# Kernel optimization log

Hardware: AMD Instinct MI355X
Metric: run time of the kernel (lower is better)

The kernel has to match this reference:

```python
import math
import jax, jax.numpy as jnp
import numpy as np

V, D, DEPTH, H, DH, FF = 32000, 1024, 4, 16, 64, 4096
B, N = 1, 2048


def setup_inputs() -> dict:
    key = jax.random.key(0)
    ks = jax.random.split(key, 8)
    s = 0.02
    return {
        "x": jax.random.randint(ks[0], (B, N), 0, V, dtype=jnp.int32),
        "token_emb": jax.random.normal(ks[1], (V, D), jnp.float32) * s,
        "attn_gamma": jnp.ones((DEPTH, D), jnp.float32),
        "w_qkv": jax.random.normal(ks[2], (DEPTH, D, 3 * H * DH), jnp.float32) * s,
        "w_attn_out": jax.random.normal(ks[3], (DEPTH, H * DH, D), jnp.float32) * s,
        "ff_gamma": jnp.ones((DEPTH, D), jnp.float32),
        "w_ff1": jax.random.normal(ks[4], (DEPTH, D, FF), jnp.float32) * s,
        "b_ff1": jnp.zeros((DEPTH, FF), jnp.float32),
        "w_ff2": jax.random.normal(ks[5], (DEPTH, FF, D), jnp.float32) * s,
        "b_ff2": jnp.zeros((DEPTH, D), jnp.float32),
        "final_gamma": jnp.ones((D,), jnp.float32),
        "w_logits": jax.random.normal(ks[6], (D, V), jnp.float32) * s,
    }


def rms_norm(x, gamma):
    # F.normalize(x, dim=-1) * sqrt(D) * gamma
    norm = jnp.sqrt(jnp.sum(x * x, axis=-1, keepdims=True))
    return x / jnp.maximum(norm, 1e-12) * (x.shape[-1] ** 0.5) * gamma


def rope_cos_sin(n, dh, dtype):
    # lucidrains rotary-embedding-torch default: interleaved pairs
    inv_freq = 1.0 / (10000.0 ** (jnp.arange(0, dh, 2, dtype=jnp.float32) / dh))
    freqs = jnp.arange(n, dtype=jnp.float32)[:, None] * inv_freq[None, :]  # [n, dh/2]
    freqs = jnp.repeat(freqs, 2, axis=-1)  # [n, dh]
    return jnp.cos(freqs).astype(dtype), jnp.sin(freqs).astype(dtype)


def rotate_half(x):
    x1 = x[..., 0::2]
    x2 = x[..., 1::2]
    return jnp.stack((-x2, x1), axis=-1).reshape(x.shape)


def apply_rope(t, cos, sin):
    # t: [b, h, n, dh]; cos/sin: [n, dh]
    return t * cos[None, None] + rotate_half(t) * sin[None, None]


def decoder_forward(x, token_emb, attn_gamma, w_qkv, w_attn_out, ff_gamma,
                    w_ff1, b_ff1, w_ff2, b_ff2, final_gamma, w_logits):
    b, n = x.shape
    h = token_emb[x]  # [b, n, D]
    cos, sin = rope_cos_sin(n, DH, h.dtype)
    causal = jnp.triu(jnp.ones((n, n), bool), k=1)
    scale = DH ** -0.5
    neg = -jnp.finfo(h.dtype).max
    for l in range(DEPTH):
        # attention block
        xn = rms_norm(h, attn_gamma[l])
        qkv = xn @ w_qkv[l]  # [b, n, 3*H*DH]
        qkv = qkv.reshape(b, n, 3, H, DH).transpose(2, 0, 3, 1, 4)  # [3, b, H, n, DH]
        q, k, v = qkv[0], qkv[1], qkv[2]
        q = apply_rope(q, cos, sin)
        k = apply_rope(k, cos, sin)
        sim = jnp.einsum('bhid,bhjd->bhij', q, k) * scale
        sim = jnp.where(causal, neg, sim)
        attn = jax.nn.softmax(sim, axis=-1)
        out = jnp.einsum('bhij,bhjd->bhid', attn, v)
        out = out.transpose(0, 2, 1, 3).reshape(b, n, H * DH) @ w_attn_out[l]
        h = h + out
        # feedforward block
        fn = rms_norm(h, ff_gamma[l])
        ff = jax.nn.gelu(fn @ w_ff1[l] + b_ff1[l], approximate=False) @ w_ff2[l] + b_ff2[l]
        h = h + ff
    return rms_norm(h, final_gamma) @ w_logits


def reference(x, token_emb, attn_gamma, w_qkv, w_attn_out, ff_gamma,
              w_ff1, b_ff1, w_ff2, b_ff2, final_gamma, w_logits):
    return decoder_forward(x, token_emb, attn_gamma, w_qkv, w_attn_out, ff_gamma,
                           w_ff1, b_ff1, w_ff2, b_ff2, final_gamma, w_logits)
```

## Files before the change

### kernel.cpp

```cpp
#include <hip/hip_runtime.h>
#include <math.h>


#define NSEQ 2048
#define DMODEL 1024
#define NH 16
#define DHEAD 64
#define FFD 4096
#define VOC 32000
#define NLAYER 4

typedef unsigned short u16;
typedef short bf16x8 __attribute__((ext_vector_type(8)));
typedef float f32x4 __attribute__((ext_vector_type(4)));

__device__ __forceinline__ u16 f2bf(float f) {
  unsigned int u = __builtin_bit_cast(unsigned int, f);
  u += 0x7fffu + ((u >> 16) & 1u);
  return (u16)(u >> 16);
}

__device__ __forceinline__ void gload16(const void* g, void* l) {
  __builtin_amdgcn_global_load_lds((__attribute__((address_space(1))) void*)g,
                                   (__attribute__((address_space(3))) void*)l,
                                   16, 0, 0);
}

__device__ __forceinline__ f32x4 mfma16x32(bf16x8 a, bf16x8 b, f32x4 c) {
  return __builtin_amdgcn_mfma_f32_16x16x32_bf16(a, b, c, 0, 0, 0);
}


__global__ __launch_bounds__(256) void k_embed(const int* __restrict__ x,
                                               const float* __restrict__ emb,
                                               float* __restrict__ h) {
  const int n = blockIdx.x, t = threadIdx.x;
  const int tok = x[n];
  reinterpret_cast<float4*>(h + (size_t)n * DMODEL)[t] =
      reinterpret_cast<const float4*>(emb + (size_t)tok * DMODEL)[t];
}

__global__ void k_rope(float* __restrict__ ct, float* __restrict__ st) {
  const int n = blockIdx.x, p = threadIdx.x;
  const double inv = exp(-(double)(2 * p) / 64.0 * log(10000.0));
  const double a = (double)n * inv;
  ct[n * 32 + p] = (float)cos(a);
  st[n * 32 + p] = (float)sin(a);
}

__global__ __launch_bounds__(256) void k_transpose(const float* __restrict__ in0,
                                                   u16* __restrict__ out0,
                                                   int K, int Nc,
                                                   size_t ls_in, size_t ls_out) {
  const float* in = in0 + blockIdx.z * ls_in;
  u16* out = out0 + blockIdx.z * ls_out;
  __shared__ float tile[64][65];
  const int kb = blockIdx.x * 64, nb = blockIdx.y * 64;
  const int tr = threadIdx.x >> 4;
  const int tc = threadIdx.x & 15;
#pragma unroll
  for (int r = 0; r < 64; r += 16) {
    const float4 v = *reinterpret_cast<const float4*>(
        &in[(size_t)(kb + r + tr) * Nc + nb + tc * 4]);
    tile[r + tr][tc * 4 + 0] = v.x;
    tile[r + tr][tc * 4 + 1] = v.y;
    tile[r + tr][tc * 4 + 2] = v.z;
    tile[r + tr][tc * 4 + 3] = v.w;
  }
  __syncthreads();
#pragma unroll
  for (int r = 0; r < 64; r += 16) {
    const int n = r + tr;
    ushort4 o;
    o.x = f2bf(tile[tc * 4 + 0][n]);
    o.y = f2bf(tile[tc * 4 + 1][n]);
    o.z = f2bf(tile[tc * 4 + 2][n]);
    o.w = f2bf(tile[tc * 4 + 3][n]);
    *reinterpret_cast<ushort4*>(&out[(size_t)(nb + n) * K + kb + tc * 4]) = o;
  }
}

__global__ __launch_bounds__(256) void k_rmsnorm(const float* __restrict__ h,
                                                 const float* __restrict__ gamma,
                                                 u16* __restrict__ out) {
  __shared__ float red[4];
  const int n = blockIdx.x, t = threadIdx.x;
  const float4 v = reinterpret_cast<const float4*>(h + (size_t)n * DMODEL)[t];
  float ss = v.x * v.x + v.y * v.y + v.z * v.z + v.w * v.w;
#pragma unroll
  for (int off = 32; off; off >>= 1) ss += __shfl_down(ss, off);
  if ((t & 63) == 0) red[t >> 6] = ss;
  __syncthreads();
  const float tot = red[0] + red[1] + red[2] + red[3];
  const float inv = 32.0f / fmaxf(sqrtf(tot), 1e-12f);
  const float4 g = reinterpret_cast<const float4*>(gamma)[t];
  ushort4 o;
  o.x = f2bf(v.x * inv * g.x);
  o.y = f2bf(v.y * inv * g.y);
  o.z = f2bf(v.z * inv * g.z);
  o.w = f2bf(v.w * inv * g.w);
  reinterpret_cast<ushort4*>(out + (size_t)n * DMODEL)[t] = o;
}

#define EPI_STORE 0
#define EPI_ADD 1
#define EPI_GELU 2
#define EPI_BIAS_ADD 3
#define EPI_QKV 4


__device__ __forceinline__ bf16x8 ldsfragT(const char* base, int row, int lg) {
  return *reinterpret_cast<const bf16x8*>(
      base + row * 64 + (((lg ^ (row & 3) ^ ((row >> 2) & 3)) & 3) << 4));
}

template <int EPI>
__global__ __launch_bounds__(256, 3) void k_gemmT(
    const u16* __restrict__ A, const u16* __restrict__ BT, int K, int Nc,
    const float* __restrict__ bias, const float* __restrict__ add,
    float* __restrict__ outf, u16* __restrict__ outb,
    u16* __restrict__ Qr, u16* __restrict__ Kr, u16* __restrict__ VT,
    const float* __restrict__ ct, const float* __restrict__ st) {
  __shared__ alignas(16) char sm[3 * 16384];
  const int nt = K >> 5;
  const int NMB = 16;
  const int nwg = gridDim.x;
  int swz = blockIdx.x;
  if ((nwg & 7) == 0) swz = (swz & 7) * (nwg >> 3) + (swz >> 3);
  const int mb = swz % NMB, nb = swz / NMB;
  const int m0 = mb * 128, n0 = nb * 128;

  const int tid = threadIdx.x, w = tid >> 6, lane = tid & 63;
  const int wr = w >> 1, wc = w & 1;
  const int lr = lane & 15, lg = lane >> 4;

  const int srow = tid >> 2;
  const int gslot = (tid & 3) ^ (srow & 3) ^ ((srow >> 2) & 3);
  const u16* ga0 = A + (size_t)(m0 + srow) * K + gslot * 8;
  const u16* ga1 = A + (size_t)(m0 + 64 + srow) * K + gslot * 8;
  const u16* gb0 = BT + (size_t)(n0 + srow) * K + gslot * 8;
  const u16* gb1 = BT + (size_t)(n0 + 64 + srow) * K + gslot * 8;
  const int ldOff = tid * 16;

#define GT_STAGE(b)                                    \
  {                                                    \
    gload16(ga0, sm + (b) * 16384 + ldOff);            \
    gload16(ga1, sm + (b) * 16384 + 4096 + ldOff);     \
    gload16(gb0, sm + (b) * 16384 + 8192 + ldOff);     \
    gload16(gb1, sm + (b) * 16384 + 12288 + ldOff);    \
    ga0 += 32; ga1 += 32; gb0 += 32; gb1 += 32;        \
  }

  GT_STAGE(0)
  GT_STAGE(1)
  asm volatile("s_waitcnt vmcnt(4)" ::: "memory");
  __builtin_amdgcn_s_barrier();

  f32x4 acc[4][4] = {};
  int cur = 0, nx2 = 2;
  for (int t = 0; t < nt; ++t) {
    const char* Ab = sm + cur * 16384;
    const char* Bb = Ab + 8192;
    const bool pf = (t + 2 < nt);
    bf16x8 af[4], bf[4];
#pragma unroll
    for (int i = 0; i < 4; ++i) {
      af[i] = ldsfragT(Ab, wr * 64 + i * 16 + lr, lg);
      bf[i] = ldsfragT(Bb, wc * 64 + i * 16 + lr, lg);
    }
    if (pf) GT_STAGE(nx2)
    __builtin_amdgcn_s_setprio(1);
#pragma unroll
    for (int mi = 0; mi < 4; ++mi)
#pragma unroll
      for (int nj = 0; nj < 4; ++nj)
        acc[mi][nj] = mfma16x32(af[mi], bf[nj], acc[mi][nj]);
    __builtin_amdgcn_s_setprio(0);
    if (t + 1 < nt) {
      __builtin_amdgcn_sched_barrier(0);
      if (pf) asm volatile("s_waitcnt vmcnt(4)" ::: "memory");
      else    asm volatile("s_waitcnt vmcnt(0)" ::: "memory");
      __builtin_amdgcn_s_barrier();
      __builtin_amdgcn_sched_barrier(0);
    }
    cur = (cur == 2) ? 0 : cur + 1;
    nx2 = (nx2 == 2) ? 0 : nx2 + 1;
  }
#undef GT_STAGE

  if (EPI == EPI_QKV) {
    const int which = n0 >> 10;
    const int hh = ((n0 & 1023) >> 6) + wc;
#pragma unroll
    for (int mi = 0; mi < 4; ++mi) {
#pragma unroll
      for (int nj = 0; nj < 4; ++nj) {
        const int d = nj * 16 + lr;
#pragma unroll
        for (int r = 0; r < 4; ++r) {
          const int row = m0 + wr * 64 + mi * 16 + lg * 4 + r;
          const float v = acc[mi][nj][r];
          if (which == 2) {
            VT[((size_t)hh * DHEAD + d) * NSEQ + row] = f2bf(v);
          } else {
            const float part = __shfl_xor(v, 1);
            const float sgn = (d & 1) ? 1.0f : -1.0f;
            const float c = ct[row * 32 + (d >> 1)];
            const float s_ = st[row * 32 + (d >> 1)];
            const u16 o = f2bf(v * c + sgn * part * s_);
            u16* dst = (which == 0) ? Qr : Kr;
            dst[((size_t)hh * NSEQ + row) * DHEAD + d] = o;
          }
        }
      }
    }
    return;
  }
#pragma unroll
  for (int mi = 0; mi < 4; ++mi) {
#pragma unroll
    for (int nj = 0; nj < 4; ++nj) {
      const int col = n0 + wc * 64 + nj * 16 + lr;
#pragma unroll
      for (int r = 0; r < 4; ++r) {
        const int row = m0 + wr * 64 + mi * 16 + lg * 4 + r;
        const size_t idx = (size_t)row * Nc + col;
        float v = acc[mi][nj][r];
        if (EPI == EPI_GELU) {
          v += bias[col];
          v = 0.5f * v * (1.0f + erff(v * 0.70710678118654752f));
          outb[idx] = f2bf(v);
        } else if (EPI == EPI_ADD) {
          outf[idx] = v + add[idx];
        } else if (EPI == EPI_BIAS_ADD) {
          outf[idx] = v + bias[col] + add[idx];
        } else {
          outf[idx] = v;
        }
      }
    }
  }
}

__global__ __launch_bounds__(256) void k_attn(const u16* __restrict__ Qr,
                                              const u16* __restrict__ Kr,
                                              const u16* __restrict__ VT,
                                              u16* __restrict__ O) {
  __shared__ alignas(16) u16 Pl[4][16 * 32];
  const int hh = blockIdx.y;
  const int w = threadIdx.x >> 6, lane = threadIdx.x & 63;
  const int lr = lane & 15, lg = lane >> 4;
  const int q0 = blockIdx.x * 64 + w * 16;
  const u16* Qh = Qr + (size_t)hh * NSEQ * DHEAD;
  const u16* Kh = Kr + (size_t)hh * NSEQ * DHEAD;
  const u16* Vh = VT + (size_t)hh * DHEAD * NSEQ;
  u16* Pw = Pl[w];

  const bf16x8 aq0 = *reinterpret_cast<const bf16x8*>(Qh + (q0 + lr) * DHEAD + lg * 8);
  const bf16x8 aq1 = *reinterpret_cast<const bf16x8*>(Qh + (q0 + lr) * DHEAD + 32 + lg * 8);

  f32x4 o0 = {}, o1 = {}, o2 = {}, o3 = {};
  float m[4], l[4];
#pragma unroll
  for (int r = 0; r < 4; ++r) { m[r] = -1e30f; l[r] = 0.0f; }

  const int jend = q0 + 15;
  for (int j0 = 0; j0 <= jend; j0 += 32) {
    f32x4 s0 = {}, s1 = {};
    {
      bf16x8 bk;
      bk = *reinterpret_cast<const bf16x8*>(Kh + (j0 + lr) * DHEAD + lg * 8);
      s0 = mfma16x32(aq0, bk, s0);
      bk = *reinterpret_cast<const bf16x8*>(Kh + (j0 + lr) * DHEAD + 32 + lg * 8);
      s0 = mfma16x32(aq1, bk, s0);
      bk = *reinterpret_cast<const bf16x8*>(Kh + (j0 + 16 + lr) * DHEAD + lg * 8);
      s1 = mfma16x32(aq0, bk, s1);
      bk = *reinterpret_cast<const bf16x8*>(Kh + (j0 + 16 + lr) * DHEAD + 32 + lg * 8);
      s1 = mfma16x32(aq1, bk, s1);
    }
    float sv0[4], sv1[4], pm[4];
#pragma unroll
    for (int r = 0; r < 4; ++r) {
      const int irow = q0 + lg * 4 + r;
      sv0[r] = (j0 + lr > irow) ? -1e30f : s0[r] * 0.125f;
      sv1[r] = (j0 + 16 + lr > irow) ? -1e30f : s1[r] * 0.125f;
      pm[r] = fmaxf(sv0[r], sv1[r]);
    }
#pragma unroll
    for (int off = 1; off < 16; off <<= 1)
#pragma unroll
      for (int r = 0; r < 4; ++r) pm[r] = fmaxf(pm[r], __shfl_xor(pm[r], off));
    float p0[4], p1[4], rs[4];
    f32x4 fv;
#pragma unroll
    for (int r = 0; r < 4; ++r) {
      const float mn = fmaxf(m[r], pm[r]);
      fv[r] = __expf(m[r] - mn);
      m[r] = mn;
      p0[r] = __expf(sv0[r] - mn);
      p1[r] = __expf(sv1[r] - mn);
      rs[r] = p0[r] + p1[r];
    }
#pragma unroll
    for (int off = 1; off < 16; off <<= 1)
#pragma unroll
      for (int r = 0; r < 4; ++r) rs[r] += __shfl_xor(rs[r], off);
#pragma unroll
    for (int r = 0; r < 4; ++r) l[r] = l[r] * fv[r] + rs[r];
    o0 *= fv; o1 *= fv; o2 *= fv; o3 *= fv;

#pragma unroll
    for (int r = 0; r < 4; ++r) {
      Pw[(lg * 4 + r) * 32 + lr] = f2bf(p0[r]);
      Pw[(lg * 4 + r) * 32 + 16 + lr] = f2bf(p1[r]);
    }
    const bf16x8 pa = *reinterpret_cast<const bf16x8*>(Pw + lr * 32 + lg * 8);
    const u16* vb = Vh + j0 + lg * 8;
    o0 = mfma16x32(pa, *reinterpret_cast<const bf16x8*>(vb + (0 + lr) * NSEQ), o0);
    o1 = mfma16x32(pa, *reinterpret_cast<const bf16x8*>(vb + (16 + lr) * NSEQ), o1);
    o2 = mfma16x32(pa, *reinterpret_cast<const bf16x8*>(vb + (32 + lr) * NSEQ), o2);
    o3 = mfma16x32(pa, *reinterpret_cast<const bf16x8*>(vb + (48 + lr) * NSEQ), o3);
  }

#pragma unroll
  for (int r = 0; r < 4; ++r) {
    const int row = q0 + lg * 4 + r;
    const float invl = 1.0f / l[r];
    u16* orow = O + (size_t)row * DMODEL + hh * DHEAD;
    orow[0 * 16 + lr] = f2bf(o0[r] * invl);
    orow[1 * 16 + lr] = f2bf(o1[r] * invl);
    orow[2 * 16 + lr] = f2bf(o2[r] * invl);
    orow[3 * 16 + lr] = f2bf(o3[r] * invl);
  }
}


extern "C" void kernel_launch(void* const* d_in, const int* in_sizes, int n_in,
                              void* d_out, int out_size, void* d_ws, size_t ws_size,
                              hipStream_t stream) {
  (void)in_sizes; (void)n_in;
  const int* x = (const int*)d_in[0];
  const float* emb = (const float*)d_in[1];
  const float* attn_gamma = (const float*)d_in[2];
  const float* w_qkv = (const float*)d_in[3];
  const float* w_attn_out = (const float*)d_in[4];
  const float* ff_gamma = (const float*)d_in[5];
  const float* w_ff1 = (const float*)d_in[6];
  const float* b_ff1 = (const float*)d_in[7];
  const float* w_ff2 = (const float*)d_in[8];
  const float* b_ff2 = (const float*)d_in[9];
  const float* final_gamma = (const float*)d_in[10];
  const float* w_logits = (const float*)d_in[11];
  float* out = (float*)d_out;

  const size_t EARLY_NEED = 176ull << 20;
  const size_t FINAL_NEED = 72ull << 20;
  char* earlyBase;
  char* finalBase;
  if (ws_size >= EARLY_NEED + FINAL_NEED) {
    earlyBase = (char*)d_ws;
    finalBase = (char*)d_ws + EARLY_NEED;
  } else if (ws_size >= FINAL_NEED && (size_t)out_size * 4 >= EARLY_NEED) {
    earlyBase = (char*)d_out;
    finalBase = (char*)d_ws;
  } else {
    return;
  }
  size_t eoff = 0, foff = 0;
  auto ealloc = [&](size_t b) { void* p = earlyBase + eoff; eoff += (b + 255) & ~(size_t)255; return p; };
  auto falloc = [&](size_t b) { void* p = finalBase + foff; foff += (b + 255) & ~(size_t)255; return p; };

  u16* wqkvT = (u16*)ealloc((size_t)NLAYER * 3072 * DMODEL * 2);
  u16* wattnT = (u16*)ealloc((size_t)NLAYER * DMODEL * DMODEL * 2);
  u16* wff1T = (u16*)ealloc((size_t)NLAYER * FFD * DMODEL * 2);
  u16* wff2T = (u16*)ealloc((size_t)NLAYER * DMODEL * FFD * 2);
  float* h = (float*)ealloc((size_t)NSEQ * DMODEL * 4);
  u16* Qr = (u16*)ealloc((size_t)NH * NSEQ * DHEAD * 2);
  u16* Kr = (u16*)ealloc((size_t)NH * NSEQ * DHEAD * 2);
  u16* VTb = (u16*)ealloc((size_t)NH * NSEQ * DHEAD * 2);
  u16* Ob = (u16*)ealloc((size_t)NSEQ * DMODEL * 2);
  u16* ff1b = (u16*)ealloc((size_t)NSEQ * FFD * 2);
  float* ct = (float*)ealloc((size_t)NSEQ * 32 * 4);
  float* st = (float*)ealloc((size_t)NSEQ * 32 * 4);
  u16* wlogT = (u16*)falloc((size_t)VOC * DMODEL * 2);
  u16* xn = (u16*)falloc((size_t)NSEQ * DMODEL * 2);

  k_rope<<<dim3(NSEQ), dim3(32), 0, stream>>>(ct, st);
  k_transpose<<<dim3(16, 48, NLAYER), 256, 0, stream>>>(
      w_qkv, wqkvT, DMODEL, 3072, (size_t)DMODEL * 3072, (size_t)3072 * DMODEL);
  k_transpose<<<dim3(16, 16, NLAYER), 256, 0, stream>>>(
      w_attn_out, wattnT, DMODEL, DMODEL, (size_t)DMODEL * DMODEL, (size_t)DMODEL * DMODEL);
  k_transpose<<<dim3(16, 64, NLAYER), 256, 0, stream>>>(
      w_ff1, wff1T, DMODEL, FFD, (size_t)DMODEL * FFD, (size_t)FFD * DMODEL);
  k_transpose<<<dim3(64, 16, NLAYER), 256, 0, stream>>>(
      w_ff2, wff2T, FFD, DMODEL, (size_t)FFD * DMODEL, (size_t)DMODEL * FFD);
  k_transpose<<<dim3(16, 500, 1), 256, 0, stream>>>(
      w_logits, wlogT, DMODEL, VOC, 0, 0);

  k_embed<<<dim3(NSEQ), 256, 0, stream>>>(x, emb, h);

  for (int lyr = 0; lyr < NLAYER; ++lyr) {
    k_rmsnorm<<<dim3(NSEQ), 256, 0, stream>>>(h, attn_gamma + (size_t)lyr * DMODEL, xn);
    k_gemmT<EPI_QKV><<<dim3(16 * 24), 256, 0, stream>>>(
        xn, wqkvT + (size_t)lyr * 3072 * DMODEL, DMODEL, 3072,
        nullptr, nullptr, nullptr, nullptr, Qr, Kr, VTb, ct, st);
    k_attn<<<dim3(NSEQ / 64, NH), 256, 0, stream>>>(Qr, Kr, VTb, Ob);
    k_gemmT<EPI_ADD><<<dim3(16 * 8), 256, 0, stream>>>(
        Ob, wattnT + (size_t)lyr * DMODEL * DMODEL, DMODEL, DMODEL,
        nullptr, h, h, nullptr, nullptr, nullptr, nullptr, nullptr, nullptr);
    k_rmsnorm<<<dim3(NSEQ), 256, 0, stream>>>(h, ff_gamma + (size_t)lyr * DMODEL, xn);
    k_gemmT<EPI_GELU><<<dim3(16 * 32), 256, 0, stream>>>(
        xn, wff1T + (size_t)lyr * FFD * DMODEL, DMODEL, FFD,
        b_ff1 + (size_t)lyr * FFD, nullptr, nullptr, ff1b,
        nullptr, nullptr, nullptr, nullptr, nullptr);
    k_gemmT<EPI_BIAS_ADD><<<dim3(16 * 8), 256, 0, stream>>>(
        ff1b, wff2T + (size_t)lyr * DMODEL * FFD, FFD, DMODEL,
        b_ff2 + (size_t)lyr * DMODEL, h, h, nullptr,
        nullptr, nullptr, nullptr, nullptr, nullptr);
  }

  k_rmsnorm<<<dim3(NSEQ), 256, 0, stream>>>(h, final_gamma, xn);
  k_gemmT<EPI_STORE><<<dim3(16 * 250), 256, 0, stream>>>(
      xn, wlogT, DMODEL, VOC,
      nullptr, nullptr, out, nullptr, nullptr, nullptr, nullptr, nullptr, nullptr);
}
```

Measured before the change: 1.374 ms.

## Retile GEMMs: 64-row tiles for narrow GEMMs, 128x256 tiles for wide ones

The GEMM kernel is templated on the M tile size. The two N=1024 GEMMs (attention-out and ff2) now use 64x128 tiles, doubling the workgroup count from 128 to 256 so the 256 CUs are better filled. A new 128x256 tile kernel is used for ff1 and the logits GEMM, raising operand reuse per LDS load. The cost is more LDS and more accumulator registers in the wide kernel, which now declares launch_bounds(256,2) and may run at lower occupancy.

```diff
diff --git a/kernel.cpp b/kernel.cpp
--- a/kernel.cpp
+++ b/kernel.cpp
@@ -28,6 +28,14 @@
 
 __device__ __forceinline__ f32x4 mfma16x32(bf16x8 a, bf16x8 b, f32x4 c) {
   return __builtin_amdgcn_mfma_f32_16x16x32_bf16(a, b, c, 0, 0, 0);
+}
+
+template <int N>
+__device__ __forceinline__ void waitvm() {
+  if constexpr (N == 0) asm volatile("s_waitcnt vmcnt(0)" ::: "memory");
+  else if constexpr (N == 3) asm volatile("s_waitcnt vmcnt(3)" ::: "memory");
+  else if constexpr (N == 4) asm volatile("s_waitcnt vmcnt(4)" ::: "memory");
+  else if constexpr (N == 6) asm volatile("s_waitcnt vmcnt(6)" ::: "memory");
 }
 
 
@@ -108,27 +116,29 @@
 #define EPI_BIAS_ADD 3
 #define EPI_QKV 4
 
-
 __device__ __forceinline__ bf16x8 ldsfragT(const char* base, int row, int lg) {
   return *reinterpret_cast<const bf16x8*>(
       base + row * 64 + (((lg ^ (row & 3) ^ ((row >> 2) & 3)) & 3) << 4));
 }
 
-template <int EPI>
-__global__ __launch_bounds__(256, 3) void k_gemmT(
+template <int EPI, int BM>
+__global__ __launch_bounds__(256) void k_gemmT(
     const u16* __restrict__ A, const u16* __restrict__ BT, int K, int Nc,
-    const float* __restrict__ bias, const float* __restrict__ add,
+    int NMB, const float* __restrict__ bias, const float* __restrict__ add,
     float* __restrict__ outf, u16* __restrict__ outb,
     u16* __restrict__ Qr, u16* __restrict__ Kr, u16* __restrict__ VT,
     const float* __restrict__ ct, const float* __restrict__ st) {
-  __shared__ alignas(16) char sm[3 * 16384];
+  constexpr int MFR = BM / 32;
+  constexpr int ABYTES = BM * 64;
+  constexpr int BUFB = ABYTES + 8192;
+  constexpr int NLD = (BM == 128) ? 4 : 3;
+  __shared__ alignas(16) char sm[3 * BUFB];
   const int nt = K >> 5;
-  const int NMB = 16;
   const int nwg = gridDim.x;
   int swz = blockIdx.x;
   if ((nwg & 7) == 0) swz = (swz & 7) * (nwg >> 3) + (swz >> 3);
   const int mb = swz % NMB, nb = swz / NMB;
-  const int m0 = mb * 128, n0 = nb * 128;
+  const int m0 = mb * BM, n0 = nb * 128;
 
   const int tid = threadIdx.x, w = tid >> 6, lane = tid & 63;
   const int wr = w >> 1, wc = w & 1;
@@ -137,68 +147,69 @@
   const int srow = tid >> 2;
   const int gslot = (tid & 3) ^ (srow & 3) ^ ((srow >> 2) & 3);
   const u16* ga0 = A + (size_t)(m0 + srow) * K + gslot * 8;
-  const u16* ga1 = A + (size_t)(m0 + 64 + srow) * K + gslot * 8;
+  const u16* ga1 = A + (size_t)(m0 + (BM == 128 ? 64 : 0) + srow) * K + gslot * 8;
   const u16* gb0 = BT + (size_t)(n0 + srow) * K + gslot * 8;
   const u16* gb1 = BT + (size_t)(n0 + 64 + srow) * K + gslot * 8;
   const int ldOff = tid * 16;
 
-#define GT_STAGE(b)                                    \
-  {                                                    \
-    gload16(ga0, sm + (b) * 16384 + ldOff);            \
-    gload16(ga1, sm + (b) * 16384 + 4096 + ldOff);     \
-    gload16(gb0, sm + (b) * 16384 + 8192 + ldOff);     \
-    gload16(gb1, sm + (b) * 16384 + 12288 + ldOff);    \
-    ga0 += 32; ga1 += 32; gb0 += 32; gb1 += 32;        \
-  }
-
-  GT_STAGE(0)
-  GT_STAGE(1)
-  asm volatile("s_waitcnt vmcnt(4)" ::: "memory");
+  auto stage = [&](int b) {
+    char* base = sm + b * BUFB;
+    gload16(ga0, base + ldOff);
+    if constexpr (BM == 128) gload16(ga1, base + 4096 + ldOff);
+    gload16(gb0, base + ABYTES + ldOff);
+    gload16(gb1, base + ABYTES + 4096 + ldOff);
+    ga0 += 32; gb0 += 32; gb1 += 32;
+    if constexpr (BM == 128) ga1 += 32;
+  };
+
+  stage(0);
+  stage(1);
+  waitvm<NLD>();
   __builtin_amdgcn_s_barrier();
 
-  f32x4 acc[4][4] = {};
+  f32x4 acc[MFR][4] = {};
   int cur = 0, nx2 = 2;
   for (int t = 0; t < nt; ++t) {
-    const char* Ab = sm + cur * 16384;
-    const char* Bb = Ab + 8192;
+    const char* Ab = sm + cur * BUFB;
+    const char* Bb = Ab + ABYTES;
     const bool pf = (t + 2 < nt);
-    bf16x8 af[4], bf[4];
-#pragma unroll
-    for (int i = 0; i < 4; ++i) {
-      af[i] = ldsfragT(Ab, wr * 64 + i * 16 + lr, lg);
+    bf16x8 af[MFR], bf[4];
+#pragma unroll
+    for (int i = 0; i < MFR; ++i)
+      af[i] = ldsfragT(Ab, wr * (BM / 2) + i * 16 + lr, lg);
+#pragma unroll
+    for (int i = 0; i < 4; ++i)
       bf[i] = ldsfragT(Bb, wc * 64 + i * 16 + lr, lg);
-    }
-    if (pf) GT_STAGE(nx2)
+    if (pf) stage(nx2);
     __builtin_amdgcn_s_setprio(1);
 #pragma unroll
-    for (int mi = 0; mi < 4; ++mi)
+    for (int mi = 0; mi < MFR; ++mi)
 #pragma unroll
       for (int nj = 0; nj < 4; ++nj)
         acc[mi][nj] = mfma16x32(af[mi], bf[nj], acc[mi][nj]);
     __builtin_amdgcn_s_setprio(0);
     if (t + 1 < nt) {
       __builtin_amdgcn_sched_barrier(0);
-      if (pf) asm volatile("s_waitcnt vmcnt(4)" ::: "memory");
-      else    asm volatile("s_waitcnt vmcnt(0)" ::: "memory");
+      if (pf) waitvm<NLD>();
+      else    waitvm<0>();
       __builtin_amdgcn_s_barrier();
       __builtin_amdgcn_sched_barrier(0);
     }
     cur = (cur == 2) ? 0 : cur + 1;
     nx2 = (nx2 == 2) ? 0 : nx2 + 1;
   }
-#undef GT_STAGE
-
-  if (EPI == EPI_QKV) {
+
+  if constexpr (EPI == EPI_QKV) {
     const int which = n0 >> 10;
     const int hh = ((n0 & 1023) >> 6) + wc;
 #pragma unroll
-    for (int mi = 0; mi < 4; ++mi) {
+    for (int mi = 0; mi < MFR; ++mi) {
 #pragma unroll
       for (int nj = 0; nj < 4; ++nj) {
         const int d = nj * 16 + lr;
 #pragma unroll
         for (int r = 0; r < 4; ++r) {
-          const int row = m0 + wr * 64 + mi * 16 + lg * 4 + r;
+          const int row = m0 + wr * (BM / 2) + mi * 16 + lg * 4 + r;
           const float v = acc[mi][nj][r];
           if (which == 2) {
             VT[((size_t)hh * DHEAD + d) * NSEQ + row] = f2bf(v);
@@ -217,13 +228,13 @@
     return;
   }
 #pragma unroll
-  for (int mi = 0; mi < 4; ++mi) {
+  for (int mi = 0; mi < MFR; ++mi) {
 #pragma unroll
     for (int nj = 0; nj < 4; ++nj) {
       const int col = n0 + wc * 64 + nj * 16 + lr;
 #pragma unroll
       for (int r = 0; r < 4; ++r) {
-        const int row = m0 + wr * 64 + mi * 16 + lg * 4 + r;
+        const int row = m0 + wr * (BM / 2) + mi * 16 + lg * 4 + r;
         const size_t idx = (size_t)row * Nc + col;
         float v = acc[mi][nj][r];
         if (EPI == EPI_GELU) {
@@ -234,6 +245,106 @@
           outf[idx] = v + add[idx];
         } else if (EPI == EPI_BIAS_ADD) {
           outf[idx] = v + bias[col] + add[idx];
+        } else {
+          outf[idx] = v;
+        }
+      }
+    }
+  }
+}
+
+template <int EPI>
+__global__ __launch_bounds__(256, 2) void k_gemmW(
+    const u16* __restrict__ A, const u16* __restrict__ BT, int K, int Nc,
+    const float* __restrict__ bias, float* __restrict__ outf,
+    u16* __restrict__ outb) {
+  constexpr int ABYTES = 8192;
+  constexpr int BUFB = ABYTES + 16384;
+  __shared__ alignas(16) char sm[3 * BUFB];
+  const int nt = K >> 5;
+  const int NMB = 16;
+  const int nwg = gridDim.x;
+  int swz = blockIdx.x;
+  if ((nwg & 7) == 0) swz = (swz & 7) * (nwg >> 3) + (swz >> 3);
+  const int mb = swz % NMB, nb = swz / NMB;
+  const int m0 = mb * 128, n0 = nb * 256;
+
+  const int tid = threadIdx.x, w = tid >> 6, lane = tid & 63;
+  const int wr = w >> 1, wc = w & 1;
+  const int lr = lane & 15, lg = lane >> 4;
+
+  const int srow = tid >> 2;
+  const int gslot = (tid & 3) ^ (srow & 3) ^ ((srow >> 2) & 3);
+  const u16* ga0 = A + (size_t)(m0 + srow) * K + gslot * 8;
+  const u16* ga1 = A + (size_t)(m0 + 64 + srow) * K + gslot * 8;
+  const u16* gb0 = BT + (size_t)(n0 + srow) * K + gslot * 8;
+  const u16* gb1 = BT + (size_t)(n0 + 64 + srow) * K + gslot * 8;
+  const u16* gb2 = BT + (size_t)(n0 + 128 + srow) * K + gslot * 8;
+  const u16* gb3 = BT + (size_t)(n0 + 192 + srow) * K + gslot * 8;
+  const int ldOff = tid * 16;
+
+  auto stage = [&](int b) {
+    char* base = sm + b * BUFB;
+    gload16(ga0, base + ldOff);
+    gload16(ga1, base + 4096 + ldOff);
+    gload16(gb0, base + ABYTES + ldOff);
+    gload16(gb1, base + ABYTES + 4096 + ldOff);
+    gload16(gb2, base + ABYTES + 8192 + ldOff);
+    gload16(gb3, base + ABYTES + 12288 + ldOff);
+    ga0 += 32; ga1 += 32; gb0 += 32; gb1 += 32; gb2 += 32; gb3 += 32;
+  };
+
+  stage(0);
+  stage(1);
+  waitvm<6>();
+  __builtin_amdgcn_s_barrier();
+
+  f32x4 acc[4][8] = {};
+  int cur = 0, nx2 = 2;
+  for (int t = 0; t < nt; ++t) {
+    const char* Ab = sm + cur * BUFB;
+    const char* Bb = Ab + ABYTES;
+    const bool pf = (t + 2 < nt);
+    bf16x8 af[4], bf[8];
+#pragma unroll
+    for (int i = 0; i < 4; ++i)
+      af[i] = ldsfragT(Ab, wr * 64 + i * 16 + lr, lg);
+#pragma unroll
+    for (int i = 0; i < 8; ++i)
+      bf[i] = ldsfragT(Bb, wc * 128 + i * 16 + lr, lg);
+    if (pf) stage(nx2);
+    __builtin_amdgcn_s_setprio(1);
+#pragma unroll
+    for (int mi = 0; mi < 4; ++mi)
+#pragma unroll
+      for (int nj = 0; nj < 8; ++nj)
+        acc[mi][nj] = mfma16x32(af[mi], bf[nj], acc[mi][nj]);
+    __builtin_amdgcn_s_setprio(0);
+    if (t + 1 < nt) {
+      __builtin_amdgcn_sched_barrier(0);
+      if (pf) waitvm<6>();
+      else    waitvm<0>();
+      __builtin_amdgcn_s_barrier();
+      __builtin_amdgcn_sched_barrier(0);
+    }
+    cur = (cur == 2) ? 0 : cur + 1;
+    nx2 = (nx2 == 2) ? 0 : nx2 + 1;
+  }
+
+#pragma unroll
+  for (int mi = 0; mi < 4; ++mi) {
+#pragma unroll
+    for (int nj = 0; nj < 8; ++nj) {
+      const int col = n0 + wc * 128 + nj * 16 + lr;
+#pragma unroll
+      for (int r = 0; r < 4; ++r) {
+        const int row = m0 + wr * 64 + mi * 16 + lg * 4 + r;
+        const size_t idx = (size_t)row * Nc + col;
+        float v = acc[mi][nj][r];
+        if (EPI == EPI_GELU) {
+          v += bias[col];
+          v = 0.5f * v * (1.0f + erff(v * 0.70710678118654752f));
+          outb[idx] = f2bf(v);
         } else {
           outf[idx] = v;
         }
@@ -401,26 +512,24 @@
 
   for (int lyr = 0; lyr < NLAYER; ++lyr) {
     k_rmsnorm<<<dim3(NSEQ), 256, 0, stream>>>(h, attn_gamma + (size_t)lyr * DMODEL, xn);
-    k_gemmT<EPI_QKV><<<dim3(16 * 24), 256, 0, stream>>>(
-        xn, wqkvT + (size_t)lyr * 3072 * DMODEL, DMODEL, 3072,
+    k_gemmT<EPI_QKV, 128><<<dim3(16 * 24), 256, 0, stream>>>(
+        xn, wqkvT + (size_t)lyr * 3072 * DMODEL, DMODEL, 3072, 16,
         nullptr, nullptr, nullptr, nullptr, Qr, Kr, VTb, ct, st);
     k_attn<<<dim3(NSEQ / 64, NH), 256, 0, stream>>>(Qr, Kr, VTb, Ob);
-    k_gemmT<EPI_ADD><<<dim3(16 * 8), 256, 0, stream>>>(
-        Ob, wattnT + (size_t)lyr * DMODEL * DMODEL, DMODEL, DMODEL,
+    k_gemmT<EPI_ADD, 64><<<dim3(32 * 8), 256, 0, stream>>>(
+        Ob, wattnT + (size_t)lyr * DMODEL * DMODEL, DMODEL, DMODEL, 32,
         nullptr, h, h, nullptr, nullptr, nullptr, nullptr, nullptr, nullptr);
     k_rmsnorm<<<dim3(NSEQ), 256, 0, stream>>>(h, ff_gamma + (size_t)lyr * DMODEL, xn);
-    k_gemmT<EPI_GELU><<<dim3(16 * 32), 256, 0, stream>>>(
+    k_gemmW<EPI_GELU><<<dim3(16 * 16), 256, 0, stream>>>(
         xn, wff1T + (size_t)lyr * FFD * DMODEL, DMODEL, FFD,
-        b_ff1 + (size_t)lyr * FFD, nullptr, nullptr, ff1b,
-        nullptr, nullptr, nullptr, nullptr, nullptr);
-    k_gemmT<EPI_BIAS_ADD><<<dim3(16 * 8), 256, 0, stream>>>(
-        ff1b, wff2T + (size_t)lyr * DMODEL * FFD, FFD, DMODEL,
+        b_ff1 + (size_t)lyr * FFD, nullptr, ff1b);
+    k_gemmT<EPI_BIAS_ADD, 64><<<dim3(32 * 8), 256, 0, stream>>>(
+        ff1b, wff2T + (size_t)lyr * DMODEL * FFD, FFD, DMODEL, 32,
         b_ff2 + (size_t)lyr * DMODEL, h, h, nullptr,
         nullptr, nullptr, nullptr, nullptr, nullptr);
   }
 
   k_rmsnorm<<<dim3(NSEQ), 256, 0, stream>>>(h, final_gamma, xn);
-  k_gemmT<EPI_STORE><<<dim3(16 * 250), 256, 0, stream>>>(
-      xn, wlogT, DMODEL, VOC,
-      nullptr, nullptr, out, nullptr, nullptr, nullptr, nullptr, nullptr, nullptr);
-}
+  k_gemmW<EPI_STORE><<<dim3(16 * 125), 256, 0, stream>>>(
+      xn, wlogT, DMODEL, VOC, nullptr, out, nullptr);
+}
```

Measured after the change: 1.371 ms. About the same (-0.2%).

## Add 64-row GEMM tiles for N=1024 GEMMs and deepen pipeline to four stages

Applied to the files above, without the earlier changes.

Templates the GEMM on the M tile size and uses 64x128 tiles for the attention-out and FF2 projections, doubling their grid from 128 to 256 workgroups so the GPU's CUs are better filled. The LDS ring buffer grows from three to four stages, with three tiles prefetched ahead and matching vmcnt waits. The trade-offs are more LDS per block, dropping the 3-waves occupancy hint, and less B-tile reuse for the smaller tiles.

```diff
diff --git a/kernel.cpp b/kernel.cpp
--- a/kernel.cpp
+++ b/kernel.cpp
@@ -28,6 +28,15 @@
 
 __device__ __forceinline__ f32x4 mfma16x32(bf16x8 a, bf16x8 b, f32x4 c) {
   return __builtin_amdgcn_mfma_f32_16x16x32_bf16(a, b, c, 0, 0, 0);
+}
+
+template <int N>
+__device__ __forceinline__ void waitvm() {
+  if constexpr (N == 0) asm volatile("s_waitcnt vmcnt(0)" ::: "memory");
+  else if constexpr (N == 3) asm volatile("s_waitcnt vmcnt(3)" ::: "memory");
+  else if constexpr (N == 4) asm volatile("s_waitcnt vmcnt(4)" ::: "memory");
+  else if constexpr (N == 6) asm volatile("s_waitcnt vmcnt(6)" ::: "memory");
+  else if constexpr (N == 8) asm volatile("s_waitcnt vmcnt(8)" ::: "memory");
 }
 
 
@@ -108,27 +117,29 @@
 #define EPI_BIAS_ADD 3
 #define EPI_QKV 4
 
-
 __device__ __forceinline__ bf16x8 ldsfragT(const char* base, int row, int lg) {
   return *reinterpret_cast<const bf16x8*>(
       base + row * 64 + (((lg ^ (row & 3) ^ ((row >> 2) & 3)) & 3) << 4));
 }
 
-template <int EPI>
-__global__ __launch_bounds__(256, 3) void k_gemmT(
+template <int EPI, int BM>
+__global__ __launch_bounds__(256) void k_gemmT(
     const u16* __restrict__ A, const u16* __restrict__ BT, int K, int Nc,
-    const float* __restrict__ bias, const float* __restrict__ add,
+    int NMB, const float* __restrict__ bias, const float* __restrict__ add,
     float* __restrict__ outf, u16* __restrict__ outb,
     u16* __restrict__ Qr, u16* __restrict__ Kr, u16* __restrict__ VT,
     const float* __restrict__ ct, const float* __restrict__ st) {
-  __shared__ alignas(16) char sm[3 * 16384];
+  constexpr int MFR = BM / 32;
+  constexpr int ABYTES = BM * 64;
+  constexpr int BUFB = ABYTES + 8192;
+  constexpr int SL = (BM == 128) ? 4 : 3;
+  __shared__ alignas(16) char sm[4 * BUFB];
   const int nt = K >> 5;
-  const int NMB = 16;
   const int nwg = gridDim.x;
   int swz = blockIdx.x;
   if ((nwg & 7) == 0) swz = (swz & 7) * (nwg >> 3) + (swz >> 3);
   const int mb = swz % NMB, nb = swz / NMB;
-  const int m0 = mb * 128, n0 = nb * 128;
+  const int m0 = mb * BM, n0 = nb * 128;
 
   const int tid = threadIdx.x, w = tid >> 6, lane = tid & 63;
   const int wr = w >> 1, wc = w & 1;
@@ -137,68 +148,69 @@
   const int srow = tid >> 2;
   const int gslot = (tid & 3) ^ (srow & 3) ^ ((srow >> 2) & 3);
   const u16* ga0 = A + (size_t)(m0 + srow) * K + gslot * 8;
-  const u16* ga1 = A + (size_t)(m0 + 64 + srow) * K + gslot * 8;
+  const u16* ga1 = A + (size_t)(m0 + (BM == 128 ? 64 : 0) + srow) * K + gslot * 8;
   const u16* gb0 = BT + (size_t)(n0 + srow) * K + gslot * 8;
   const u16* gb1 = BT + (size_t)(n0 + 64 + srow) * K + gslot * 8;
   const int ldOff = tid * 16;
 
-#define GT_STAGE(b)                                    \
-  {                                                    \
-    gload16(ga0, sm + (b) * 16384 + ldOff);            \
-    gload16(ga1, sm + (b) * 16384 + 4096 + ldOff);     \
-    gload16(gb0, sm + (b) * 16384 + 8192 + ldOff);     \
-    gload16(gb1, sm + (b) * 16384 + 12288 + ldOff);    \
-    ga0 += 32; ga1 += 32; gb0 += 32; gb1 += 32;        \
-  }
-
-  GT_STAGE(0)
-  GT_STAGE(1)
-  asm volatile("s_waitcnt vmcnt(4)" ::: "memory");
+  auto stage = [&](int b) {
+    char* base = sm + b * BUFB;
+    gload16(ga0, base + ldOff);
+    if constexpr (BM == 128) gload16(ga1, base + 4096 + ldOff);
+    gload16(gb0, base + ABYTES + ldOff);
+    gload16(gb1, base + ABYTES + 4096 + ldOff);
+    ga0 += 32; gb0 += 32; gb1 += 32;
+    if constexpr (BM == 128) ga1 += 32;
+  };
+
+  stage(0);
+  stage(1);
+  stage(2);
+  waitvm<2 * SL>();
   __builtin_amdgcn_s_barrier();
 
-  f32x4 acc[4][4] = {};
-  int cur = 0, nx2 = 2;
+  f32x4 acc[MFR][4] = {};
+  int cur = 0;
   for (int t = 0; t < nt; ++t) {
-    const char* Ab = sm + cur * 16384;
-    const char* Bb = Ab + 8192;
-    const bool pf = (t + 2 < nt);
-    bf16x8 af[4], bf[4];
-#pragma unroll
-    for (int i = 0; i < 4; ++i) {
-      af[i] = ldsfragT(Ab, wr * 64 + i * 16 + lr, lg);
+    const char* Ab = sm + cur * BUFB;
+    const char* Bb = Ab + ABYTES;
+    bf16x8 af[MFR], bf[4];
+#pragma unroll
+    for (int i = 0; i < MFR; ++i)
+      af[i] = ldsfragT(Ab, wr * (BM / 2) + i * 16 + lr, lg);
+#pragma unroll
+    for (int i = 0; i < 4; ++i)
       bf[i] = ldsfragT(Bb, wc * 64 + i * 16 + lr, lg);
-    }
-    if (pf) GT_STAGE(nx2)
+    if (t + 3 < nt) stage((cur + 3) & 3);
     __builtin_amdgcn_s_setprio(1);
 #pragma unroll
-    for (int mi = 0; mi < 4; ++mi)
+    for (int mi = 0; mi < MFR; ++mi)
 #pragma unroll
       for (int nj = 0; nj < 4; ++nj)
         acc[mi][nj] = mfma16x32(af[mi], bf[nj], acc[mi][nj]);
     __builtin_amdgcn_s_setprio(0);
     if (t + 1 < nt) {
       __builtin_amdgcn_sched_barrier(0);
-      if (pf) asm volatile("s_waitcnt vmcnt(4)" ::: "memory");
-      else    asm volatile("s_waitcnt vmcnt(0)" ::: "memory");
+      if (t + 3 < nt)      waitvm<2 * SL>();
+      else if (t + 2 < nt) waitvm<SL>();
+      else                 waitvm<0>();
       __builtin_amdgcn_s_barrier();
       __builtin_amdgcn_sched_barrier(0);
     }
-    cur = (cur == 2) ? 0 : cur + 1;
-    nx2 = (nx2 == 2) ? 0 : nx2 + 1;
-  }
-#undef GT_STAGE
-
-  if (EPI == EPI_QKV) {
+    cur = (cur + 1) & 3;
+  }
+
+  if constexpr (EPI == EPI_QKV) {
     const int which = n0 >> 10;
     const int hh = ((n0 & 1023) >> 6) + wc;
 #pragma unroll
-    for (int mi = 0; mi < 4; ++mi) {
+    for (int mi = 0; mi < MFR; ++mi) {
 #pragma unroll
       for (int nj = 0; nj < 4; ++nj) {
         const int d = nj * 16 + lr;
 #pragma unroll
         for (int r = 0; r < 4; ++r) {
-          const int row = m0 + wr * 64 + mi * 16 + lg * 4 + r;
+          const int row = m0 + wr * (BM / 2) + mi * 16 + lg * 4 + r;
           const float v = acc[mi][nj][r];
           if (which == 2) {
             VT[((size_t)hh * DHEAD + d) * NSEQ + row] = f2bf(v);
@@ -217,13 +229,13 @@
     return;
   }
 #pragma unroll
-  for (int mi = 0; mi < 4; ++mi) {
+  for (int mi = 0; mi < MFR; ++mi) {
 #pragma unroll
     for (int nj = 0; nj < 4; ++nj) {
       const int col = n0 + wc * 64 + nj * 16 + lr;
 #pragma unroll
       for (int r = 0; r < 4; ++r) {
-        const int row = m0 + wr * 64 + mi * 16 + lg * 4 + r;
+        const int row = m0 + wr * (BM / 2) + mi * 16 + lg * 4 + r;
         const size_t idx = (size_t)row * Nc + col;
         float v = acc[mi][nj][r];
         if (EPI == EPI_GELU) {
@@ -401,26 +413,26 @@
 
   for (int lyr = 0; lyr < NLAYER; ++lyr) {
     k_rmsnorm<<<dim3(NSEQ), 256, 0, stream>>>(h, attn_gamma + (size_t)lyr * DMODEL, xn);
-    k_gemmT<EPI_QKV><<<dim3(16 * 24), 256, 0, stream>>>(
-        xn, wqkvT + (size_t)lyr * 3072 * DMODEL, DMODEL, 3072,
+    k_gemmT<EPI_QKV, 128><<<dim3(16 * 24), 256, 0, stream>>>(
+        xn, wqkvT + (size_t)lyr * 3072 * DMODEL, DMODEL, 3072, 16,
         nullptr, nullptr, nullptr, nullptr, Qr, Kr, VTb, ct, st);
     k_attn<<<dim3(NSEQ / 64, NH), 256, 0, stream>>>(Qr, Kr, VTb, Ob);
-    k_gemmT<EPI_ADD><<<dim3(16 * 8), 256, 0, stream>>>(
-        Ob, wattnT + (size_t)lyr * DMODEL * DMODEL, DMODEL, DMODEL,
+    k_gemmT<EPI_ADD, 64><<<dim3(32 * 8), 256, 0, stream>>>(
+        Ob, wattnT + (size_t)lyr * DMODEL * DMODEL, DMODEL, DMODEL, 32,
         nullptr, h, h, nullptr, nullptr, nullptr, nullptr, nullptr, nullptr);
     k_rmsnorm<<<dim3(NSEQ), 256, 0, stream>>>(h, ff_gamma + (size_t)lyr * DMODEL, xn);
-    k_gemmT<EPI_GELU><<<dim3(16 * 32), 256, 0, stream>>>(
-        xn, wff1T + (size_t)lyr * FFD * DMODEL, DMODEL, FFD,
+    k_gemmT<EPI_GELU, 128><<<dim3(16 * 32), 256, 0, stream>>>(
+        xn, wff1T + (size_t)lyr * FFD * DMODEL, DMODEL, FFD, 16,
         b_ff1 + (size_t)lyr * FFD, nullptr, nullptr, ff1b,
         nullptr, nullptr, nullptr, nullptr, nullptr);
-    k_gemmT<EPI_BIAS_ADD><<<dim3(16 * 8), 256, 0, stream>>>(
-        ff1b, wff2T + (size_t)lyr * DMODEL * FFD, FFD, DMODEL,
+    k_gemmT<EPI_BIAS_ADD, 64><<<dim3(32 * 8), 256, 0, stream>>>(
+        ff1b, wff2T + (size_t)lyr * DMODEL * FFD, FFD, DMODEL, 32,
         b_ff2 + (size_t)lyr * DMODEL, h, h, nullptr,
         nullptr, nullptr, nullptr, nullptr, nullptr);
   }
 
   k_rmsnorm<<<dim3(NSEQ), 256, 0, stream>>>(h, final_gamma, xn);
-  k_gemmT<EPI_STORE><<<dim3(16 * 250), 256, 0, stream>>>(
-      xn, wlogT, DMODEL, VOC,
+  k_gemmT<EPI_STORE, 128><<<dim3(16 * 250), 256, 0, stream>>>(
+      xn, wlogT, DMODEL, VOC, 16,
       nullptr, nullptr, out, nullptr, nullptr, nullptr, nullptr, nullptr, nullptr);
 }
```

Result: faster. 1.313 ms (-4.4%).
